# Kernel tuning notes

Measured on AMD Instinct MI355X. Metric: run time of the kernel, lower is better.

## Reference

```python
import jax, jax.numpy as jnp
import numpy as np

N_NODES = 50000
N_EDGES = 800000
IN_DIM = 256
HIDDEN = 32
HEADS = 4
OUT_DIM = 64


def setup_inputs() -> dict:
    key = jax.random.key(0)
    k1, k2, k3, k4, k5, k6, k7 = jax.random.split(key, 7)
    h = jax.random.normal(k1, (N_NODES, IN_DIM), dtype=jnp.float32)
    src = jax.random.randint(k2, (N_EDGES,), 0, N_NODES, dtype=jnp.int32)
    dst = jax.random.randint(k3, (N_EDGES,), 0, N_NODES, dtype=jnp.int32)
    # xavier_normal with relu gain, per-head weights
    gain = float(np.sqrt(2.0))
    W1 = gain * jnp.sqrt(2.0 / (IN_DIM + HIDDEN)) * jax.random.normal(k4, (HEADS, IN_DIM, HIDDEN), dtype=jnp.float32)
    a1 = gain * jnp.sqrt(2.0 / (2 * HIDDEN + 1)) * jax.random.normal(k5, (HEADS, 2 * HIDDEN), dtype=jnp.float32)
    W2 = gain * jnp.sqrt(2.0 / (HIDDEN * HEADS + OUT_DIM)) * jax.random.normal(k6, (1, HIDDEN * HEADS, OUT_DIM), dtype=jnp.float32)
    a2 = gain * jnp.sqrt(2.0 / (2 * OUT_DIM + 1)) * jax.random.normal(k7, (1, 2 * OUT_DIM), dtype=jnp.float32)
    return {"h": h, "src": src, "dst": dst, "W1": W1, "a1": a1, "W2": W2, "a2": a2}


def _gat_layer(x, src, dst, W, a):
    # x: [N, in], W: [H, in, d], a: [H, 2d]
    N = x.shape[0]
    d = W.shape[-1]
    z = jnp.einsum('ni,hio->nho', x, W)                    # [N, H, d]
    a_s, a_d = a[:, :d], a[:, d:]
    es = jnp.einsum('nho,ho->nh', z, a_s)                  # per-node src score
    ed = jnp.einsum('nho,ho->nh', z, a_d)                  # per-node dst score
    e = jax.nn.leaky_relu(es[src] + ed[dst])               # [E, H]
    # segment (per-destination) softmax over incoming edges
    emax = jax.ops.segment_max(e, dst, num_segments=N)     # [N, H]
    ex = jnp.exp(e - emax[dst])
    denom = jax.ops.segment_sum(ex, dst, num_segments=N)   # [N, H]
    alpha = ex / denom[dst]                                # [E, H]
    # scatter weighted sum of source feats back to destinations
    out = jax.ops.segment_sum(alpha[:, :, None] * z[src], dst, num_segments=N)  # [N, H, d]
    return out.reshape(N, -1)


def reference(h, src, dst, W1, a1, W2, a2):
    h1 = jax.nn.elu(_gat_layer(h, src, dst, W1, a1))       # [N, HEADS*HIDDEN]
    return _gat_layer(h1, src, dst, W2, a2)                # [N, OUT_DIM]
```

## Files before the change

### kernel.cpp

```cpp
#include <hip/hip_runtime.h>
#include <hip/hip_bf16.h>
#include <math.h>

#define N_NODES 50000
#define N_EDGES 800000
#define IN_DIM 256
#define HID 32
#define HEADS 4
#define OUT_DIM 64

#define SCAN_CHUNK 1024
#define SCAN_BLOCKS ((N_NODES + SCAN_CHUNK - 1) / SCAN_CHUNK)
#define HIST_BLOCKS ((N_EDGES + 255) / 256)
#define MBLK ((N_NODES + 63) / 64)

typedef __attribute__((ext_vector_type(8))) short bf16x8;
typedef __attribute__((ext_vector_type(4))) float f32x4;

__device__ __forceinline__ float lrelu(float e) { return e > 0.f ? e : 0.01f * e; }
__device__ __forceinline__ float bflo(unsigned u) { return __uint_as_float(u << 16); }
__device__ __forceinline__ float bfhi(unsigned u) { return __uint_as_float(u & 0xffff0000u); }

__device__ __forceinline__ unsigned short rne_bf16(float x) {
    unsigned u = __float_as_uint(x);
    unsigned r = u + 0x7fffu + ((u >> 16) & 1u);
    return (unsigned short)(r >> 16);
}

__device__ __forceinline__ void splitf(float x, short& hi, short& lo) {
    unsigned u = __float_as_uint(x);
    unsigned short h = (unsigned short)(u >> 16);
    float hf = __uint_as_float(((unsigned)h) << 16);
    float l = x - hf;
    unsigned short lb = (unsigned short)(__float_as_uint(l) >> 16);
    hi = (short)h;
    lo = (short)lb;
}


__device__ __forceinline__ void prep_body(int k, int c,
        const float* __restrict__ W1, const float* __restrict__ a1,
        const float* __restrict__ W2, const float* __restrict__ a2,
        unsigned short* __restrict__ B1h, unsigned short* __restrict__ B1l,
        unsigned short* __restrict__ B2h, unsigned short* __restrict__ B2l) {
    if (c < 144) {
        float val = 0.f;
        if (c < 128) {
            val = W1[(size_t)(c >> 5) * IN_DIM * HID + (size_t)k * HID + (c & 31)];
        } else if (c < 136) {
            int j = c - 128;
            int hd = (j < 4) ? j : (j - 4);
            int off = (j < 4) ? 0 : HID;
            const float* Wp = W1 + (size_t)hd * IN_DIM * HID + (size_t)k * HID;
            const float* ap = a1 + hd * 2 * HID + off;
            float s = 0.f;
            for (int o = 0; o < HID; o++) s += Wp[o] * ap[o];
            val = s;
        }
        unsigned short hi = rne_bf16(val);
        float hf = __uint_as_float(((unsigned)hi) << 16);
        unsigned short lo = rne_bf16(val - hf);
        int s_ = k >> 5, q = (k >> 3) & 3, j8 = k & 7;
        int nt = c >> 4, L = q * 16 + (c & 15);
        size_t idx = (((size_t)s_ * 9 + nt) * 64 + L) * 8 + j8;
        B1h[idx] = hi;
        B1l[idx] = lo;
    } else if (c >= 160 && c < 240 && k < 128) {
        int c2 = c - 160;
        int ck = (2 * (k >> 5) + (k & 1)) * 16 + ((k & 31) >> 1);
        float val = 0.f;
        if (c2 < 64) {
            val = W2[(size_t)ck * OUT_DIM + c2];
        } else if (c2 < 66) {
            const float* ap = a2 + (c2 - 64) * OUT_DIM;
            const float* Wp = W2 + (size_t)ck * OUT_DIM;
            float s = 0.f;
            for (int o = 0; o < OUT_DIM; o++) s += Wp[o] * ap[o];
            val = s;
        }
        unsigned short hi = rne_bf16(val);
        float hf = __uint_as_float(((unsigned)hi) << 16);
        unsigned short lo = rne_bf16(val - hf);
        int s_ = k >> 5, q = (k >> 3) & 3, j8 = k & 7;
        int nt = c2 >> 4, L = q * 16 + (c2 & 15);
        size_t idx = (((size_t)s_ * 5 + nt) * 64 + L) * 8 + j8;
        B2h[idx] = hi;
        B2l[idx] = lo;
    }
}


__global__ void __launch_bounds__(256) prep_hist_kernel(
        const float* __restrict__ W1, const float* __restrict__ a1,
        const float* __restrict__ W2, const float* __restrict__ a2,
        unsigned short* __restrict__ B1h, unsigned short* __restrict__ B1l,
        unsigned short* __restrict__ B2h, unsigned short* __restrict__ B2l,
        const int* __restrict__ dst, int* __restrict__ count) {
    int bid = blockIdx.x;
    if (bid < 256) {
        prep_body(bid, threadIdx.x, W1, a1, W2, a2, B1h, B1l, B2h, B2l);
    } else {
        int i = (bid - 256) * 256 + threadIdx.x;
        if (i < N_EDGES) atomicAdd(&count[dst[i]], 1);
    }
}


__device__ __forceinline__ void scan1_body(int bid, int t, const int* __restrict__ count,
        int* __restrict__ rs_local, int* __restrict__ cursor,
        int* __restrict__ bs_prefix, int* sdata) {
    int base = bid * SCAN_CHUNK + t * 4;
    int v[4];
    int s = 0;
#pragma unroll
    for (int j = 0; j < 4; j++) {
        int idx = base + j;
        int x = (idx < N_NODES) ? count[idx] : 0;
        v[j] = x;
        s += x;
    }
    sdata[t] = s;
    __syncthreads();
    for (int off = 1; off < 256; off <<= 1) {
        int u = (t >= off) ? sdata[t - off] : 0;
        __syncthreads();
        sdata[t] += u;
        __syncthreads();
    }
    int excl = sdata[t] - s;
#pragma unroll
    for (int j = 0; j < 4; j++) {
        int idx = base + j;
        if (idx < N_NODES) {
            rs_local[idx] = excl;
            cursor[idx] = excl;
        }
        excl += v[j];
    }
    if (t > bid && t < SCAN_BLOCKS) atomicAdd(&bs_prefix[t], sdata[255]);
}


__device__ __forceinline__ void proj1_body(int n0, int L,
        const float* __restrict__ h, const unsigned short* __restrict__ Bh,
        const unsigned short* __restrict__ Bl, __hip_bfloat16* __restrict__ z1b,
        float* __restrict__ es1, float* __restrict__ ed1) {
    int q = L >> 4, L15 = L & 15;
    int rowA = n0 + L15;
    int rrA = rowA < N_NODES ? rowA : N_NODES - 1;
    const float* hrow = h + (size_t)rrA * IN_DIM + q * 8;

    f32x4 acc[9];
#pragma unroll
    for (int nt = 0; nt < 9; nt++) acc[nt] = (f32x4)(0.f);

    float4 x0 = *(const float4*)(hrow);
    float4 x1 = *(const float4*)(hrow + 4);

#pragma unroll
    for (int s = 0; s < 8; s++) {
        int sn = (s < 7) ? s + 1 : 7;
        float4 p0 = *(const float4*)(hrow + sn * 32);
        float4 p1 = *(const float4*)(hrow + sn * 32 + 4);

        float xs[8] = {x0.x, x0.y, x0.z, x0.w, x1.x, x1.y, x1.z, x1.w};
        bf16x8 ah, al;
#pragma unroll
        for (int j = 0; j < 8; j++) {
            short hi, lo;
            splitf(xs[j], hi, lo);
            ah[j] = hi;
            al[j] = lo;
        }

        const bf16x8* bhp = (const bf16x8*)(Bh + ((size_t)s * 9 * 64) * 8 + (size_t)L * 8);
        const bf16x8* blp = (const bf16x8*)(Bl + ((size_t)s * 9 * 64) * 8 + (size_t)L * 8);
#pragma unroll
        for (int nt = 0; nt < 9; nt++) {
            bf16x8 bh = bhp[nt * 64];
            acc[nt] = __builtin_amdgcn_mfma_f32_16x16x32_bf16(ah, bh, acc[nt], 0, 0, 0);
            acc[nt] = __builtin_amdgcn_mfma_f32_16x16x32_bf16(al, bh, acc[nt], 0, 0, 0);
        }
        {
            bf16x8 bl8 = blp[8 * 64];
            acc[8] = __builtin_amdgcn_mfma_f32_16x16x32_bf16(ah, bl8, acc[8], 0, 0, 0);
        }
        x0 = p0;
        x1 = p1;
    }

#pragma unroll
    for (int r = 0; r < 4; r++) {
        int rowc = n0 + q * 4 + r;
        if (rowc < N_NODES) {
            unsigned* zp = (unsigned*)(z1b + (size_t)rowc * 128);
#pragma unroll
            for (int hh = 0; hh < 4; hh++) {
                unsigned wv = (unsigned)rne_bf16(acc[2 * hh][r]) |
                              ((unsigned)rne_bf16(acc[2 * hh + 1][r]) << 16);
                zp[hh * 16 + L15] = wv;
            }
            if (L15 < 4) es1[rowc * HEADS + L15] = acc[8][r];
            else if (L15 < 8) ed1[rowc * HEADS + (L15 - 4)] = acc[8][r];
        }
    }
}


__global__ void __launch_bounds__(256) scan_proj1_kernel(
        const float* __restrict__ h, const unsigned short* __restrict__ Bh,
        const unsigned short* __restrict__ Bl, __hip_bfloat16* __restrict__ z1b,
        float* __restrict__ es1, float* __restrict__ ed1,
        const int* __restrict__ count, int* __restrict__ rs_local,
        int* __restrict__ cursor, int* __restrict__ bs_prefix) {
    if (blockIdx.x < SCAN_BLOCKS) {
        __shared__ int sdata[256];
        scan1_body(blockIdx.x, threadIdx.x, count, rs_local, cursor, bs_prefix, sdata);
        return;
    }
    int wave = threadIdx.x >> 6;
    int L = threadIdx.x & 63;
    int n0 = (blockIdx.x - SCAN_BLOCKS) * 64 + wave * 16;
    proj1_body(n0, L, h, Bh, Bl, z1b, es1, ed1);
}


__global__ void scatter_kernel(const int* __restrict__ src, const int* __restrict__ dst,
                               int* __restrict__ cursor, const int* __restrict__ bs_prefix,
                               int* __restrict__ esrc) {
    int i = blockIdx.x * blockDim.x + threadIdx.x;
    if (i < N_EDGES) {
        int d = dst[i];
        int pos = atomicAdd(&cursor[d], 1);
        esrc[pos + bs_prefix[d >> 10]] = src[i];
    }
}


__global__ void __launch_bounds__(256) agg1_kernel(
        const __hip_bfloat16* __restrict__ z1b, const float* __restrict__ es1,
        const float* __restrict__ ed1, const int* __restrict__ rs_local,
        const int* __restrict__ bs_prefix, const int* __restrict__ count,
        const int* __restrict__ esrc, __hip_bfloat16* __restrict__ h1b) {
    int v = blockIdx.x * 4 + (threadIdx.x >> 6);
    int L = threadIdx.x & 63;
    int sub = L >> 4;
    int c16 = L & 15;
    int hd = c16 >> 2;
    int beg = rs_local[v] + bs_prefix[v >> 10], deg = count[v];
    float edv = ed1[v * HEADS + hd];
    const int* ep = esrc + beg;
    float lacc = 0.f;
    float acc[8];
#pragma unroll
    for (int i = 0; i < 8; i++) acc[i] = 0.f;
    const uint4* zq = (const uint4*)z1b;

    for (int j0 = 0; j0 < deg; j0 += 32) {
        int se[8];
        uint4 u[8];
        float ev[8];
#pragma unroll
        for (int g = 0; g < 8; g++) {
            if (j0 + g * 4 < deg) {
                int e = j0 + g * 4 + sub;
                se[g] = ep[(e < deg) ? e : 0];
            }
        }
#pragma unroll
        for (int g = 0; g < 8; g++) {
            if (j0 + g * 4 < deg) {
                u[g] = zq[(size_t)se[g] * 16 + c16];
                ev[g] = es1[se[g] * HEADS + hd];
            }
        }
#pragma unroll
        for (int g = 0; g < 8; g++) {
            if (j0 + g * 4 < deg) {
                bool val = (j0 + g * 4 + sub) < deg;
                float q = val ? __expf(lrelu(ev[g] + edv)) : 0.f;
                lacc += q;
                acc[0] = fmaf(q, bflo(u[g].x), acc[0]);
                acc[1] = fmaf(q, bfhi(u[g].x), acc[1]);
                acc[2] = fmaf(q, bflo(u[g].y), acc[2]);
                acc[3] = fmaf(q, bfhi(u[g].y), acc[3]);
                acc[4] = fmaf(q, bflo(u[g].z), acc[4]);
                acc[5] = fmaf(q, bfhi(u[g].z), acc[5]);
                acc[6] = fmaf(q, bflo(u[g].w), acc[6]);
                acc[7] = fmaf(q, bfhi(u[g].w), acc[7]);
            }
        }
    }
    lacc += __shfl_xor(lacc, 1);
    lacc += __shfl_xor(lacc, 2);
    lacc += __shfl_xor(lacc, 16);
    lacc += __shfl_xor(lacc, 32);
    lacc *= 0.25f;
#pragma unroll
    for (int i = 0; i < 8; i++) {
        acc[i] += __shfl_xor(acc[i], 16);
        acc[i] += __shfl_xor(acc[i], 32);
    }
    if (L < 16) {
        float inv = (deg > 0) ? 1.f / lacc : 0.f;
        unsigned w[4];
#pragma unroll
        for (int i = 0; i < 4; i++) {
            float r0 = acc[2 * i] * inv;
            float r1 = acc[2 * i + 1] * inv;
            r0 = r0 > 0.f ? r0 : __expf(r0) - 1.f;
            r1 = r1 > 0.f ? r1 : __expf(r1) - 1.f;
            w[i] = (unsigned)rne_bf16(r0) | ((unsigned)rne_bf16(r1) << 16);
        }
        uint4* dstp = (uint4*)(h1b + (size_t)v * 128 + c16 * 8);
        *dstp = make_uint4(w[0], w[1], w[2], w[3]);
    }
}


__global__ void __launch_bounds__(256) proj2_mfma(
        const __hip_bfloat16* __restrict__ h1b, const unsigned short* __restrict__ Bh,
        const unsigned short* __restrict__ Bl, __hip_bfloat16* __restrict__ z2b,
        float* __restrict__ es2, float* __restrict__ ed2) {
    int tid = threadIdx.x;
    int wave = tid >> 6;
    int L = tid & 63;
    int q = L >> 4, L15 = L & 15;
    int n0 = blockIdx.x * 64 + wave * 16;

    int rowA = n0 + L15;
    int rrA = rowA < N_NODES ? rowA : N_NODES - 1;
    const bf16x8* hq = (const bf16x8*)(h1b + (size_t)rrA * 128);

    bf16x8 av[4];
#pragma unroll
    for (int s = 0; s < 4; s++) av[s] = hq[s * 4 + q];

    f32x4 acc[5];
#pragma unroll
    for (int nt = 0; nt < 5; nt++) acc[nt] = (f32x4)(0.f);

#pragma unroll
    for (int s = 0; s < 4; s++) {
        const bf16x8* bhp = (const bf16x8*)(Bh + ((size_t)s * 5 * 64) * 8 + (size_t)L * 8);
        const bf16x8* blp = (const bf16x8*)(Bl + ((size_t)s * 5 * 64) * 8 + (size_t)L * 8);
#pragma unroll
        for (int nt = 0; nt < 5; nt++)
            acc[nt] = __builtin_amdgcn_mfma_f32_16x16x32_bf16(av[s], bhp[nt * 64], acc[nt], 0, 0, 0);
        acc[4] = __builtin_amdgcn_mfma_f32_16x16x32_bf16(av[s], blp[4 * 64], acc[4], 0, 0, 0);
    }

#pragma unroll
    for (int r = 0; r < 4; r++) {
        int rowc = n0 + q * 4 + r;
        if (rowc < N_NODES) {
#pragma unroll
            for (int nt = 0; nt < 4; nt++)
                z2b[(size_t)rowc * OUT_DIM + nt * 16 + L15] = __float2bfloat16(acc[nt][r]);
            if (L15 == 0) es2[rowc] = acc[4][r];
            else if (L15 == 1) ed2[rowc] = acc[4][r];
        }
    }
}


__global__ void __launch_bounds__(256) agg2_kernel(
        const __hip_bfloat16* __restrict__ z2b, const float* __restrict__ es2,
        const float* __restrict__ ed2, const int* __restrict__ rs_local,
        const int* __restrict__ bs_prefix, const int* __restrict__ count,
        const int* __restrict__ esrc, float* __restrict__ out) {
    int v = blockIdx.x * 4 + (threadIdx.x >> 6);
    int L = threadIdx.x & 63;
    int sub = L >> 3;
    int c8 = L & 7;
    int beg = rs_local[v] + bs_prefix[v >> 10], deg = count[v];
    float edv = ed2[v];
    const int* ep = esrc + beg;
    float lacc = 0.f;
    float acc[8];
#pragma unroll
    for (int i = 0; i < 8; i++) acc[i] = 0.f;
    const uint4* zq = (const uint4*)z2b;

    for (int j0 = 0; j0 < deg; j0 += 32) {
        int se[4];
        uint4 u[4];
        float ev[4];
#pragma unroll
        for (int g = 0; g < 4; g++) {
            if (j0 + g * 8 < deg) {
                int e = j0 + g * 8 + sub;
                se[g] = ep[(e < deg) ? e : 0];
            }
        }
#pragma unroll
        for (int g = 0; g < 4; g++) {
            if (j0 + g * 8 < deg) {
                u[g] = zq[(size_t)se[g] * 8 + c8];
                ev[g] = es2[se[g]];
            }
        }
#pragma unroll
        for (int g = 0; g < 4; g++) {
            if (j0 + g * 8 < deg) {
                bool val = (j0 + g * 8 + sub) < deg;
                float q = val ? __expf(lrelu(ev[g] + edv)) : 0.f;
                lacc += q;
                acc[0] = fmaf(q, bflo(u[g].x), acc[0]);
                acc[1] = fmaf(q, bfhi(u[g].x), acc[1]);
                acc[2] = fmaf(q, bflo(u[g].y), acc[2]);
                acc[3] = fmaf(q, bfhi(u[g].y), acc[3]);
                acc[4] = fmaf(q, bflo(u[g].z), acc[4]);
                acc[5] = fmaf(q, bfhi(u[g].z), acc[5]);
                acc[6] = fmaf(q, bflo(u[g].w), acc[6]);
                acc[7] = fmaf(q, bfhi(u[g].w), acc[7]);
            }
        }
    }
    lacc += __shfl_xor(lacc, 8);
    lacc += __shfl_xor(lacc, 16);
    lacc += __shfl_xor(lacc, 32);
#pragma unroll
    for (int i = 0; i < 8; i++) {
        acc[i] += __shfl_xor(acc[i], 8);
        acc[i] += __shfl_xor(acc[i], 16);
        acc[i] += __shfl_xor(acc[i], 32);
    }
    if (L < 8) {
        float inv = (deg > 0) ? 1.f / lacc : 0.f;
        float4 r0, r1;
#pragma unroll
        for (int i = 0; i < 8; i++) {
            float r = acc[i] * inv;
            if (i < 4) (&r0.x)[i] = r;
            else (&r1.x)[i - 4] = r;
        }
        float* dstp = out + (size_t)v * OUT_DIM + c8 * 8;
        *(float4*)dstp = r0;
        *(float4*)(dstp + 4) = r1;
    }
}


extern "C" void kernel_launch(void* const* d_in, const int* in_sizes, int n_in,
                              void* d_out, int out_size, void* d_ws, size_t ws_size,
                              hipStream_t stream) {
    const float* h  = (const float*)d_in[0];
    const int* src  = (const int*)d_in[1];
    const int* dst  = (const int*)d_in[2];
    const float* W1 = (const float*)d_in[3];
    const float* a1 = (const float*)d_in[4];
    const float* W2 = (const float*)d_in[5];
    const float* a2 = (const float*)d_in[6];
    float* out = (float*)d_out;

    char* w = (char*)d_ws;
    size_t off = 0;
    auto alloc = [&](size_t bytes) {
        void* p = w + off;
        off = (off + bytes + 255) & ~(size_t)255;
        return p;
    };
    __hip_bfloat16* z1b = (__hip_bfloat16*)alloc((size_t)N_NODES * 128 * 2);
    float* es1 = (float*)alloc((size_t)N_NODES * HEADS * 4);
    float* ed1 = (float*)alloc((size_t)N_NODES * HEADS * 4);
    __hip_bfloat16* h1b = (__hip_bfloat16*)alloc((size_t)N_NODES * 128 * 2);
    __hip_bfloat16* z2b = (__hip_bfloat16*)alloc((size_t)N_NODES * OUT_DIM * 2);
    float* es2 = (float*)alloc((size_t)N_NODES * 4);
    float* ed2 = (float*)alloc((size_t)N_NODES * 4);
    int* count     = (int*)alloc((size_t)(N_NODES + 64) * 4);
    int* bs_prefix = count + N_NODES;
    int* rs_local  = (int*)alloc((size_t)N_NODES * 4);
    int* cursor    = (int*)alloc((size_t)N_NODES * 4);
    int* esrc      = (int*)alloc((size_t)N_EDGES * 4);
    unsigned short* Bf1h = (unsigned short*)alloc((size_t)8 * 9 * 64 * 8 * 2);
    unsigned short* Bf1l = (unsigned short*)alloc((size_t)8 * 9 * 64 * 8 * 2);
    unsigned short* Bf2h = (unsigned short*)alloc((size_t)4 * 5 * 64 * 8 * 2);
    unsigned short* Bf2l = (unsigned short*)alloc((size_t)4 * 5 * 64 * 8 * 2);

    hipMemsetAsync(count, 0, (size_t)(N_NODES + 64) * 4, stream);

    prep_hist_kernel<<<256 + HIST_BLOCKS, 256, 0, stream>>>(
        W1, a1, W2, a2, Bf1h, Bf1l, Bf2h, Bf2l, dst, count);

    scan_proj1_kernel<<<SCAN_BLOCKS + MBLK, 256, 0, stream>>>(
        h, Bf1h, Bf1l, z1b, es1, ed1, count, rs_local, cursor, bs_prefix);

    scatter_kernel<<<HIST_BLOCKS, 256, 0, stream>>>(src, dst, cursor, bs_prefix, esrc);

    agg1_kernel<<<N_NODES / 4, 256, 0, stream>>>(
        z1b, es1, ed1, rs_local, bs_prefix, count, esrc, h1b);
    proj2_mfma<<<MBLK, 256, 0, stream>>>(h1b, Bf2h, Bf2l, z2b, es2, ed2);
    agg2_kernel<<<N_NODES / 4, 256, 0, stream>>>(
        z2b, es2, ed2, rs_local, bs_prefix, count, esrc, out);
}
```

Before: 264.0 us.

## Record per-edge rank in histogram, scatter without atomics, fold memset into prep

Result: faster. 214.7 us (median of 2 runs) (-18.7%).

```diff
diff --git a/kernel.cpp b/kernel.cpp
--- a/kernel.cpp
+++ b/kernel.cpp
@@ -90,54 +90,15 @@
 }
 
 
-__global__ void __launch_bounds__(256) prep_hist_kernel(
+__global__ void __launch_bounds__(256) prep_kernel(
         const float* __restrict__ W1, const float* __restrict__ a1,
         const float* __restrict__ W2, const float* __restrict__ a2,
         unsigned short* __restrict__ B1h, unsigned short* __restrict__ B1l,
         unsigned short* __restrict__ B2h, unsigned short* __restrict__ B2l,
-        const int* __restrict__ dst, int* __restrict__ count) {
-    int bid = blockIdx.x;
-    if (bid < 256) {
-        prep_body(bid, threadIdx.x, W1, a1, W2, a2, B1h, B1l, B2h, B2l);
-    } else {
-        int i = (bid - 256) * 256 + threadIdx.x;
-        if (i < N_EDGES) atomicAdd(&count[dst[i]], 1);
-    }
-}
-
-
-__device__ __forceinline__ void scan1_body(int bid, int t, const int* __restrict__ count,
-        int* __restrict__ rs_local, int* __restrict__ cursor,
-        int* __restrict__ bs_prefix, int* sdata) {
-    int base = bid * SCAN_CHUNK + t * 4;
-    int v[4];
-    int s = 0;
-#pragma unroll
-    for (int j = 0; j < 4; j++) {
-        int idx = base + j;
-        int x = (idx < N_NODES) ? count[idx] : 0;
-        v[j] = x;
-        s += x;
-    }
-    sdata[t] = s;
-    __syncthreads();
-    for (int off = 1; off < 256; off <<= 1) {
-        int u = (t >= off) ? sdata[t - off] : 0;
-        __syncthreads();
-        sdata[t] += u;
-        __syncthreads();
-    }
-    int excl = sdata[t] - s;
-#pragma unroll
-    for (int j = 0; j < 4; j++) {
-        int idx = base + j;
-        if (idx < N_NODES) {
-            rs_local[idx] = excl;
-            cursor[idx] = excl;
-        }
-        excl += v[j];
-    }
-    if (t > bid && t < SCAN_BLOCKS) atomicAdd(&bs_prefix[t], sdata[255]);
+        int* __restrict__ count) {
+    int gid = blockIdx.x * 256 + threadIdx.x;
+    if (gid < N_NODES + 64) count[gid] = 0;
+    prep_body(blockIdx.x, threadIdx.x, W1, a1, W2, a2, B1h, B1l, B2h, B2l);
 }
 
 
@@ -207,32 +168,66 @@
 }
 
 
-__global__ void __launch_bounds__(256) scan_proj1_kernel(
+__global__ void __launch_bounds__(256) proj1_hist_kernel(
         const float* __restrict__ h, const unsigned short* __restrict__ Bh,
         const unsigned short* __restrict__ Bl, __hip_bfloat16* __restrict__ z1b,
         float* __restrict__ es1, float* __restrict__ ed1,
+        const int* __restrict__ dst, int* __restrict__ count,
+        int* __restrict__ rank) {
+    int bid = blockIdx.x;
+    if (bid < MBLK) {
+        int wave = threadIdx.x >> 6;
+        int L = threadIdx.x & 63;
+        proj1_body(bid * 64 + wave * 16, L, h, Bh, Bl, z1b, es1, ed1);
+    } else {
+        int i = (bid - MBLK) * 256 + threadIdx.x;
+        if (i < N_EDGES) rank[i] = atomicAdd(&count[dst[i]], 1);
+    }
+}
+
+
+__global__ void __launch_bounds__(256) scan_kernel(
         const int* __restrict__ count, int* __restrict__ rs_local,
-        int* __restrict__ cursor, int* __restrict__ bs_prefix) {
-    if (blockIdx.x < SCAN_BLOCKS) {
-        __shared__ int sdata[256];
-        scan1_body(blockIdx.x, threadIdx.x, count, rs_local, cursor, bs_prefix, sdata);
-        return;
-    }
-    int wave = threadIdx.x >> 6;
-    int L = threadIdx.x & 63;
-    int n0 = (blockIdx.x - SCAN_BLOCKS) * 64 + wave * 16;
-    proj1_body(n0, L, h, Bh, Bl, z1b, es1, ed1);
+        int* __restrict__ bs_prefix) {
+    __shared__ int sdata[256];
+    int bid = blockIdx.x;
+    int t = threadIdx.x;
+    int base = bid * SCAN_CHUNK + t * 4;
+    int v[4];
+    int s = 0;
+#pragma unroll
+    for (int j = 0; j < 4; j++) {
+        int idx = base + j;
+        int x = (idx < N_NODES) ? count[idx] : 0;
+        v[j] = x;
+        s += x;
+    }
+    sdata[t] = s;
+    __syncthreads();
+    for (int off = 1; off < 256; off <<= 1) {
+        int u = (t >= off) ? sdata[t - off] : 0;
+        __syncthreads();
+        sdata[t] += u;
+        __syncthreads();
+    }
+    int excl = sdata[t] - s;
+#pragma unroll
+    for (int j = 0; j < 4; j++) {
+        int idx = base + j;
+        if (idx < N_NODES) rs_local[idx] = excl;
+        excl += v[j];
+    }
+    if (t > bid && t < SCAN_BLOCKS) atomicAdd(&bs_prefix[t], sdata[255]);
 }
 
 
 __global__ void scatter_kernel(const int* __restrict__ src, const int* __restrict__ dst,
-                               int* __restrict__ cursor, const int* __restrict__ bs_prefix,
-                               int* __restrict__ esrc) {
+                               const int* __restrict__ rank, const int* __restrict__ rs_local,
+                               const int* __restrict__ bs_prefix, int* __restrict__ esrc) {
     int i = blockIdx.x * blockDim.x + threadIdx.x;
     if (i < N_EDGES) {
         int d = dst[i];
-        int pos = atomicAdd(&cursor[d], 1);
-        esrc[pos + bs_prefix[d >> 10]] = src[i];
+        esrc[rs_local[d] + bs_prefix[d >> 10] + rank[i]] = src[i];
     }
 }
 
@@ -471,22 +466,21 @@
     int* count     = (int*)alloc((size_t)(N_NODES + 64) * 4);
     int* bs_prefix = count + N_NODES;
     int* rs_local  = (int*)alloc((size_t)N_NODES * 4);
-    int* cursor    = (int*)alloc((size_t)N_NODES * 4);
+    int* rank      = (int*)alloc((size_t)N_EDGES * 4);
     int* esrc      = (int*)alloc((size_t)N_EDGES * 4);
     unsigned short* Bf1h = (unsigned short*)alloc((size_t)8 * 9 * 64 * 8 * 2);
     unsigned short* Bf1l = (unsigned short*)alloc((size_t)8 * 9 * 64 * 8 * 2);
     unsigned short* Bf2h = (unsigned short*)alloc((size_t)4 * 5 * 64 * 8 * 2);
     unsigned short* Bf2l = (unsigned short*)alloc((size_t)4 * 5 * 64 * 8 * 2);
 
-    hipMemsetAsync(count, 0, (size_t)(N_NODES + 64) * 4, stream);
-
-    prep_hist_kernel<<<256 + HIST_BLOCKS, 256, 0, stream>>>(
-        W1, a1, W2, a2, Bf1h, Bf1l, Bf2h, Bf2l, dst, count);
-
-    scan_proj1_kernel<<<SCAN_BLOCKS + MBLK, 256, 0, stream>>>(
-        h, Bf1h, Bf1l, z1b, es1, ed1, count, rs_local, cursor, bs_prefix);
-
-    scatter_kernel<<<HIST_BLOCKS, 256, 0, stream>>>(src, dst, cursor, bs_prefix, esrc);
+    prep_kernel<<<256, 256, 0, stream>>>(W1, a1, W2, a2, Bf1h, Bf1l, Bf2h, Bf2l, count);
+
+    proj1_hist_kernel<<<MBLK + HIST_BLOCKS, 256, 0, stream>>>(
+        h, Bf1h, Bf1l, z1b, es1, ed1, dst, count, rank);
+
+    scan_kernel<<<SCAN_BLOCKS, 256, 0, stream>>>(count, rs_local, bs_prefix);
+
+    scatter_kernel<<<HIST_BLOCKS, 256, 0, stream>>>(src, dst, rank, rs_local, bs_prefix, esrc);
 
     agg1_kernel<<<N_NODES / 4, 256, 0, stream>>>(
         z1b, es1, ed1, rs_local, bs_prefix, count, esrc, h1b);
```
